# Kernel tuning notes

Measured on AMD Instinct MI355X. Metric: run time of the kernel, lower is better.

## Reference

```python
import jax, jax.numpy as jnp
import numpy as np

N_NODES = 100000
N_EDGES = 1000000
N_GRAPHS = 4096
F_IN = 9
H = 64


def setup_inputs() -> dict:
    key = jax.random.key(0)
    ks = jax.random.split(key, 12)
    x = jax.random.normal(ks[0], (N_NODES, F_IN), dtype=jnp.float32)
    edge_index = jax.random.randint(ks[1], (2, N_EDGES), 0, N_NODES, dtype=jnp.int64)
    batch = jnp.sort(jax.random.randint(ks[2], (N_NODES,), 0, N_GRAPHS, dtype=jnp.int64))
    def lin(k, fan_in, fan_out):
        s = 1.0 / np.sqrt(fan_in)
        return jax.random.uniform(k, (fan_in, fan_out), jnp.float32, -s, s)
    return {
        "x": x, "edge_index": edge_index, "batch": batch,
        "W1": lin(ks[3], F_IN, H), "b1": jnp.zeros((H,), jnp.float32),
        "W2": lin(ks[4], H, H),    "b2": jnp.zeros((H,), jnp.float32),
        "W3": lin(ks[5], H, H),    "b3": jnp.zeros((H,), jnp.float32),
        "W4": lin(ks[6], H, H),    "b4": jnp.zeros((H,), jnp.float32),
        "Wout": lin(ks[7], H, 1),  "bout": jnp.zeros((1,), jnp.float32),
    }


def reference(x, edge_index, batch, W1, b1, W2, b2, W3, b3, W4, b4, Wout, bout):
    N = x.shape[0]
    loops = jnp.arange(N, dtype=edge_index.dtype)
    src = jnp.concatenate([edge_index[0], loops])  # messages flow src -> dst (PyG source_to_target)
    dst = jnp.concatenate([edge_index[1], loops])
    # symmetric GCN normalization with self-loops: deg includes self-loop
    deg = jax.ops.segment_sum(jnp.ones_like(dst, dtype=x.dtype), dst, num_segments=N)
    dis = jax.lax.rsqrt(jnp.maximum(deg, 1.0))  # deg >= 1 thanks to self-loops
    norm = dis[src] * dis[dst]                  # [E+N]

    def gcn_conv(h, W, b):
        h = h @ W                                # transform first (PyG order)
        msgs = h[src] * norm[:, None]            # [E+N, H]
        return jax.ops.segment_sum(msgs, dst, num_segments=N) + b

    h = jax.nn.relu(gcn_conv(x, W1, b1))
    h = jax.nn.relu(gcn_conv(h, W2, b2))
    h = jax.nn.relu(gcn_conv(h, W3, b3))
    h = jax.nn.relu(gcn_conv(h, W4, b4))

    # global mean pool over graphs
    sums = jax.ops.segment_sum(h, batch, num_segments=N_GRAPHS)      # [G, H]
    counts = jax.ops.segment_sum(jnp.ones((N,), h.dtype), batch, num_segments=N_GRAPHS)
    pooled = sums / jnp.maximum(counts, 1.0)[:, None]
    return pooled @ Wout + bout                  # [G, 1]
```

## Files before the change

### kernel.cpp

```cpp
#include <hip/hip_runtime.h>
#include <hip/hip_fp16.h>


static inline size_t align256(size_t x){ return (x + 255) & ~size_t(255); }

#define CHUNK 2048
#define SCAP  3072

struct __align__(8)  h4v { __half2 a, b; };
struct __align__(16) h8v { __half2 a, b, c, d; };

typedef _Float16 f16x8 __attribute__((ext_vector_type(8)));
typedef float    f32x4 __attribute__((ext_vector_type(4)));

__global__ __launch_bounds__(256) void k_sortchunk(
    const int* __restrict__ src, const int* __restrict__ dst,
    int* __restrict__ binned, int* __restrict__ hoffC, int E){
  __shared__ int hcnt[1024];
  __shared__ int simg[CHUNK];
  int c = blockIdx.x, t = threadIdx.x;
  int e0 = c*CHUNK;
  int cnt = E - e0; if (cnt > CHUNK) cnt = CHUNK;

  for (int i = t; i < 1024; i += 256) hcnt[i] = 0;
  __syncthreads();

  int b_[8], r_[8], v_[8];
  #pragma unroll
  for (int j = 0; j < 8; j++){
    int i = t + j*256;
    if (i < cnt){
      int d = dst[e0+i];
      int s = src[e0+i];
      int b = d >> 7;
      b_[j] = b;
      r_[j] = atomicAdd(&hcnt[b], 1);
      v_[j] = (s << 7) | (d & 127);
    } else b_[j] = -1;
  }
  __syncthreads();

  int own[4];
  #pragma unroll
  for (int j = 0; j < 4; j++) own[j] = hcnt[t + j*256];
  for (int off = 1; off < 1024; off <<= 1){
    int nv[4];
    #pragma unroll
    for (int j = 0; j < 4; j++){
      int i = t + j*256;
      nv[j] = hcnt[i] + ((i >= off) ? hcnt[i-off] : 0);
    }
    __syncthreads();
    #pragma unroll
    for (int j = 0; j < 4; j++) hcnt[t + j*256] = nv[j];
    __syncthreads();
  }
  #pragma unroll
  for (int j = 0; j < 4; j++) hcnt[t + j*256] -= own[j];
  __syncthreads();

  for (int i = t; i < 783; i += 256) hoffC[c*783 + i] = hcnt[i];

  #pragma unroll
  for (int j = 0; j < 8; j++)
    if (b_[j] >= 0) simg[hcnt[b_[j]] + r_[j]] = v_[j];
  __syncthreads();

  for (int i = t; i < cnt; i += 256) binned[e0 + i] = simg[i];
}

__global__ __launch_bounds__(256) void k_bktsum(
    const int* __restrict__ hoffC, int* __restrict__ btot,
    float* __restrict__ gsum, int NC, int NBK, int G){
  __shared__ int s[256];
  int b = blockIdx.x, t = threadIdx.x;
  int gid = b*256 + t;
  if (gid < G) gsum[gid] = 0.f;
  int tot = 0;
  for (int c = t; c < NC; c += 256)
    tot += hoffC[c*783 + b + 1] - hoffC[c*783 + b];
  s[t] = tot; __syncthreads();
  for (int off = 128; off > 0; off >>= 1){
    if (t < off) s[t] += s[t+off];
    __syncthreads();
  }
  if (t == 0) btot[b] = s[0];
}

__global__ __launch_bounds__(1024) void k_bktscan(
    const int* __restrict__ btot, int* __restrict__ bbase,
    int* __restrict__ row_ptr, int NBK, int N, int E){
  __shared__ int s[1024];
  int t = threadIdx.x;
  int v = (t < NBK) ? btot[t] : 0;
  s[t] = v; __syncthreads();
  for (int off = 1; off < 1024; off <<= 1){
    int add = (t >= off) ? s[t-off] : 0; __syncthreads();
    s[t] += add; __syncthreads();
  }
  if (t < NBK) bbase[t] = s[t] - v;
  if (t == 0) row_ptr[N] = E;
}

__global__ __launch_bounds__(256) void k_gather2(
    const int* __restrict__ binned, const int* __restrict__ hoffC,
    const int* __restrict__ bbase, const float* __restrict__ x,
    int* __restrict__ row_ptr, float* __restrict__ dis,
    float* __restrict__ xs, int* __restrict__ csr, int N, int NC){
  __shared__ int lcur[128];
  __shared__ int lscan[128];
  __shared__ float ldis[128];
  __shared__ int stage[SCAP];
  __shared__ int scount;
  int b = blockIdx.x, t = threadIdx.x;
  int n0 = b << 7;
  int nn = N - n0; if (nn > 128) nn = 128;
  if (t < 128) lcur[t] = 0;
  if (t == 0) scount = 0;
  __syncthreads();
  for (int c = t; c < NC; c += 256){
    int o0 = hoffC[c*783 + b];
    int o1 = hoffC[c*783 + b + 1];
    int len = o1 - o0;
    if (len > 0){
      int base = atomicAdd(&scount, len);
      int sbase = c*CHUNK;
      for (int k = 0; k < len; k++){
        int v = binned[sbase + o0 + k];
        atomicAdd(&lcur[v & 127], 1);
        int pos = base + k;
        if (pos < SCAP) stage[pos] = v;
      }
    }
  }
  __syncthreads();
  int degv = (t < 128) ? lcur[t] : 0;
  if (t < 128) lscan[t] = degv;
  __syncthreads();
  for (int off = 1; off < 128; off <<= 1){
    int add = (t < 128 && t >= off) ? lscan[t-off] : 0;
    __syncthreads();
    if (t < 128) lscan[t] += add;
    __syncthreads();
  }
  int bb = bbase[b];
  if (t < nn){
    int row = bb + lscan[t] - degv;
    row_ptr[n0 + t] = row;
    float dv = rsqrtf((float)(degv + 1));
    dis[n0 + t] = dv;
    ldis[t] = dv;
    lcur[t] = row;
  }
  __syncthreads();
  for (int i = t; i < nn*9; i += 256)
    xs[(size_t)n0*9 + i] = x[(size_t)n0*9 + i] * ldis[i/9];
  int sc = scount;
  if (sc <= SCAP){
    for (int i = t; i < sc; i += 256){
      int v = stage[i];
      int pos = atomicAdd(&lcur[v & 127], 1);
      csr[pos] = v >> 7;
    }
  } else {
    for (int c = t; c < NC; c += 256){
      int o0 = hoffC[c*783 + b];
      int o1 = hoffC[c*783 + b + 1];
      int sbase = c*CHUNK;
      for (int k = o0; k < o1; k++){
        int v = binned[sbase + k];
        int pos = atomicAdd(&lcur[v & 127], 1);
        csr[pos] = v >> 7;
      }
    }
  }
}

__global__ void k_agg9(const float* __restrict__ xs, const float* __restrict__ dis,
                       const int* __restrict__ row_ptr, const int* __restrict__ csr,
                       float* __restrict__ xagg, int N){
  int tid = blockIdx.x*blockDim.x + threadIdx.x;
  if (tid >= N*9) return;
  int n = tid/9, f = tid - n*9;
  float dn = dis[n];
  int s0 = row_ptr[n], s1 = row_ptr[n+1];
  float a0 = xs[tid];
  float a1 = 0.f, a2 = 0.f, a3 = 0.f;
  int j = s0;
  for (; j + 3 < s1; j += 4){
    int e0 = csr[j], e1 = csr[j+1], e2 = csr[j+2], e3 = csr[j+3];
    a0 += xs[e0*9+f];
    a1 += xs[e1*9+f];
    a2 += xs[e2*9+f];
    a3 += xs[e3*9+f];
  }
  for (; j < s1; j++) a0 += xs[csr[j]*9+f];
  xagg[tid] = ((a0+a1)+(a2+a3))*dn;
}

__device__ __forceinline__ void mfma_epilogue(
    const _Float16* hlw, const f16x8 (&wf)[4][2],
    __half* __restrict__ mo, int wid, int nwaves, int N, int lane){
  int lm = lane & 15, lk = lane >> 4;
  f16x8 hb0 = *(const f16x8*)(hlw + lm*72 + lk*8);
  f16x8 hb1 = *(const f16x8*)(hlw + lm*72 + 32 + lk*8);
  int node = wid + lm*nwaves;
  bool ok = (node < N);
  __half* row = mo + (size_t)node*64;
  #pragma unroll
  for (int ft = 0; ft < 4; ft++){
    f32x4 acc = {0.f, 0.f, 0.f, 0.f};
    acc = __builtin_amdgcn_mfma_f32_16x16x32_f16(wf[ft][0], hb0, acc, 0, 0, 0);
    acc = __builtin_amdgcn_mfma_f32_16x16x32_f16(wf[ft][1], hb1, acc, 0, 0, 0);
    if (ok){
      h4v o;
      o.a = __floats2half2_rn(acc[0], acc[1]);
      o.b = __floats2half2_rn(acc[2], acc[3]);
      *(h4v*)(row + ft*16 + lk*4) = o;
    }
  }
}

#define LOAD_WFRAGS(Wn)                                                    \
  f16x8 wf[4][2];                                                          \
  { int lm_ = lane & 15, lk_ = lane >> 4;                                  \
    _Pragma("unroll") for (int ft = 0; ft < 4; ft++)                       \
    _Pragma("unroll") for (int kb = 0; kb < 2; kb++)                       \
    _Pragma("unroll") for (int j = 0; j < 8; j++)                          \
      wf[ft][kb][j] = (_Float16)Wn[(kb*32 + lk_*8 + j)*64 + ft*16 + lm_]; }

__global__ __launch_bounds__(256) void k_lin1_fused(
    const float* __restrict__ xagg, const float* __restrict__ W1,
    const float* __restrict__ b1, const float* __restrict__ dis,
    const float* __restrict__ W2, __half* __restrict__ mo, int N, int nwaves){
  __shared__ float W1l[576];
  __shared__ float b1l[64];
  __shared__ _Float16 hl[4][16*72];
  int t = threadIdx.x;
  for (int i = t; i < 576; i += 256) W1l[i] = W1[i];
  if (t < 64) b1l[t] = b1[t];
  __syncthreads();
  int lane = t & 63, w = t >> 6;
  int wid = (blockIdx.x*blockDim.x + t) >> 6;
  LOAD_WFRAGS(W2)
  _Float16* hlw = hl[w];
  for (int i = 0; i < 16; i++){
    int n = wid + i*nwaves;
    _Float16 hv = (_Float16)0.f;
    if (n < N){
      float acc = b1l[lane];
      #pragma unroll
      for (int k = 0; k < 9; k++) acc = fmaf(xagg[n*9+k], W1l[k*64+lane], acc);
      hv = (_Float16)(fmaxf(acc, 0.f) * dis[n]);
    }
    hlw[i*72 + lane] = hv;
  }
  mfma_epilogue(hlw, wf, mo, wid, nwaves, N, lane);
}

#define ACC8(g_)  do{ float2 t_;                                   \
  t_ = __half22float2((g_).a); acc0 += t_.x; acc1 += t_.y;         \
  t_ = __half22float2((g_).b); acc2 += t_.x; acc3 += t_.y;         \
  t_ = __half22float2((g_).c); acc4 += t_.x; acc5 += t_.y;         \
  t_ = __half22float2((g_).d); acc6 += t_.x; acc7 += t_.y; }while(0)

#define RED3(v)  do{ v += __shfl_xor(v, 8,64);                     \
                     v += __shfl_xor(v,16,64);                     \
                     v += __shfl_xor(v,32,64); }while(0)

#define AGG_ISSUE(n_, rp0_, rp1_, rn0_, rn1_, e0_, e1_, g0_, g1_, sf_, dn_) \
  do{                                                                      \
    int nn_ = (n_) + 2*nwaves;                                             \
    rn0_ = 0; rn1_ = 0;                                                    \
    if (nn_ < N){ rn0_ = row_ptr[nn_]; rn1_ = row_ptr[nn_+1]; }            \
    e0_ = -1; e1_ = -1;                                                    \
    if ((n_) < N){                                                         \
      sf_ = m[(size_t)(n_)*8 + q2];                                        \
      dn_ = dis[n_];                                                       \
      int j0_ = (rp0_) + sub, j1_ = (rp0_) + 8 + sub;                      \
      if (j0_ < (rp1_)) e0_ = csr[j0_];                                    \
      if (j1_ < (rp1_)) e1_ = csr[j1_];                                    \
      if (e0_ >= 0) g0_ = m[(size_t)e0_*8 + q2];                           \
      if (e1_ >= 0) g1_ = m[(size_t)e1_*8 + q2];                           \
    }                                                                      \
  }while(0)

#define AGG_ACCRED(n_, rp0_, rp1_, e0_, e1_, g0_, g1_, sf_, dn_)           \
      float acc0=0.f,acc1=0.f,acc2=0.f,acc3=0.f;                           \
      float acc4=0.f,acc5=0.f,acc6=0.f,acc7=0.f;                           \
      if (e0_ >= 0) ACC8(g0_);                                             \
      if (e1_ >= 0) ACC8(g1_);                                             \
      for (int j_ = (rp0_) + 16 + sub; j_ < (rp1_); j_ += 8){              \
        h8v gx_ = m[(size_t)csr[j_]*8 + q2]; ACC8(gx_);                    \
      }                                                                    \
      RED3(acc0); RED3(acc1); RED3(acc2); RED3(acc3);                      \
      RED3(acc4); RED3(acc5); RED3(acc6); RED3(acc7);                      \
      float2 s01=__half22float2((sf_).a), s23=__half22float2((sf_).b);     \
      float2 s45=__half22float2((sf_).c), s67=__half22float2((sf_).d);     \
      float r0 = fmaxf(fmaf(acc0 + s01.x, dn_, bb0.x), 0.f);               \
      float r1 = fmaxf(fmaf(acc1 + s01.y, dn_, bb0.y), 0.f);               \
      float r2 = fmaxf(fmaf(acc2 + s23.x, dn_, bb0.z), 0.f);               \
      float r3 = fmaxf(fmaf(acc3 + s23.y, dn_, bb0.w), 0.f);               \
      float r4 = fmaxf(fmaf(acc4 + s45.x, dn_, bb1.x), 0.f);               \
      float r5 = fmaxf(fmaf(acc5 + s45.y, dn_, bb1.y), 0.f);               \
      float r6 = fmaxf(fmaf(acc6 + s67.x, dn_, bb1.z), 0.f);               \
      float r7 = fmaxf(fmaf(acc7 + s67.y, dn_, bb1.w), 0.f);

#define AGG_REDUCE(n_, rp0_, rp1_, e0_, e1_, g0_, g1_, sf_, dn_, i_)       \
  do{                                                                      \
    if ((n_) < N){                                                         \
      AGG_ACCRED(n_, rp0_, rp1_, e0_, e1_, g0_, g1_, sf_, dn_)             \
      if (sub == 0){                                                       \
        h8v hv_;                                                           \
        hv_.a = __floats2half2_rn(r0*(dn_), r1*(dn_));                     \
        hv_.b = __floats2half2_rn(r2*(dn_), r3*(dn_));                     \
        hv_.c = __floats2half2_rn(r4*(dn_), r5*(dn_));                     \
        hv_.d = __floats2half2_rn(r6*(dn_), r7*(dn_));                     \
        *(h8v*)(hlw + (i_)*72 + q2*8) = hv_;                               \
      }                                                                    \
    } else if (sub == 0){                                                  \
      h8v z_; z_.a = __floats2half2_rn(0.f, 0.f);                          \
      z_.b = z_.a; z_.c = z_.a; z_.d = z_.a;                               \
      *(h8v*)(hlw + (i_)*72 + q2*8) = z_;                                  \
    }                                                                      \
  }while(0)

#define OUT_ISSUE(n_, rp0_, rp1_, rn0_, rn1_, e0_, e1_, g0_, g1_, sf_, dn_, bg_) \
  do{                                                                      \
    int pn_ = (n_) + nwaves;                                               \
    rn0_ = 0; rn1_ = 0;                                                    \
    if (pn_ < N){ rn0_ = row_ptr[pn_]; rn1_ = row_ptr[pn_+1]; }            \
    sf_ = m[(size_t)(n_)*8 + q2];                                          \
    dn_ = dis[n_];                                                         \
    bg_ = batch[n_];                                                       \
    e0_ = -1; e1_ = -1;                                                    \
    int j0_ = (rp0_) + sub, j1_ = (rp0_) + 8 + sub;                        \
    if (j0_ < (rp1_)) e0_ = csr[j0_];                                      \
    if (j1_ < (rp1_)) e1_ = csr[j1_];                                      \
    if (e0_ >= 0) g0_ = m[(size_t)e0_*8 + q2];                             \
    if (e1_ >= 0) g1_ = m[(size_t)e1_*8 + q2];                             \
  }while(0)

#define OUT_REDUCE(n_, rp0_, rp1_, e0_, e1_, g0_, g1_, sf_, dn_, bg_)      \
  do{                                                                      \
    float4 bb0 = b4[q2*2], bb1 = b4[q2*2+1];                               \
    float4 w0 = wo4[q2*2], w1 = wo4[q2*2+1];                               \
    AGG_ACCRED(n_, rp0_, rp1_, e0_, e1_, g0_, g1_, sf_, dn_)               \
    float p_ = r0*w0.x + r1*w0.y + r2*w0.z + r3*w0.w                       \
             + r4*w1.x + r5*w1.y + r6*w1.z + r7*w1.w;                      \
    p_ += __shfl_xor(p_,1,64); p_ += __shfl_xor(p_,2,64);                  \
    p_ += __shfl_xor(p_,4,64);                                             \
    if (lane == 0) atomicAdd(&gsum[bg_], p_);                              \
  }while(0)

__global__ __launch_bounds__(256) void k_agg_fused(
    const h8v* __restrict__ m, const float* __restrict__ dis,
    const float* __restrict__ b, const float* __restrict__ Wn,
    const int* __restrict__ row_ptr, const int* __restrict__ csr,
    __half* __restrict__ mo, int N, int nwaves){
  __shared__ _Float16 hl[4][16*72];
  int t = threadIdx.x;
  int lane = t & 63, w = t >> 6;
  int sub = lane >> 3, q2 = lane & 7;
  int wid = (blockIdx.x*blockDim.x + t) >> 6;
  _Float16* hlw = hl[w];
  const float4* b4 = (const float4*)b;
  float4 bb0 = b4[q2*2], bb1 = b4[q2*2+1];

  int nA = wid,          rA0 = 0, rA1 = 0;
  int nB = wid + nwaves, rB0 = 0, rB1 = 0;
  if (nA < N){ rA0 = row_ptr[nA]; rA1 = row_ptr[nA+1]; }
  if (nB < N){ rB0 = row_ptr[nB]; rB1 = row_ptr[nB+1]; }
  int eA0, eA1, eB0, eB1, rnA0, rnA1, rnB0, rnB1;
  h8v gA0, gA1, sfA, gB0, gB1, sfB;
  float dnA = 0.f, dnB = 0.f;
  AGG_ISSUE(nA, rA0, rA1, rnA0, rnA1, eA0, eA1, gA0, gA1, sfA, dnA);
  for (int p = 0; p < 8; p++){
    AGG_ISSUE(nB, rB0, rB1, rnB0, rnB1, eB0, eB1, gB0, gB1, sfB, dnB);
    AGG_REDUCE(nA, rA0, rA1, eA0, eA1, gA0, gA1, sfA, dnA, 2*p);
    nA += 2*nwaves; rA0 = rnA0; rA1 = rnA1;
    if (p < 7)
      AGG_ISSUE(nA, rA0, rA1, rnA0, rnA1, eA0, eA1, gA0, gA1, sfA, dnA);
    AGG_REDUCE(nB, rB0, rB1, eB0, eB1, gB0, gB1, sfB, dnB, 2*p+1);
    nB += 2*nwaves; rB0 = rnB0; rB1 = rnB1;
  }
  LOAD_WFRAGS(Wn)
  mfma_epilogue(hlw, wf, mo, wid, nwaves, N, lane);
}

__global__ __launch_bounds__(256) void k_agg64_out(
    const h8v* __restrict__ m, const float* __restrict__ dis,
    const float* __restrict__ b, const float* __restrict__ Wout,
    const int* __restrict__ batch,
    const int* __restrict__ row_ptr, const int* __restrict__ csr,
    float* gsum, int N, int nwaves){
  int lane = threadIdx.x & 63;
  int sub = lane >> 3, q2 = lane & 7;
  int wid = (blockIdx.x*blockDim.x + threadIdx.x) >> 6;
  if (wid >= N) return;
  const float4* b4 = (const float4*)b;
  const float4* wo4 = (const float4*)Wout;

  int nA = wid;
  int rA0 = row_ptr[nA], rA1 = row_ptr[nA+1];
  int rnA0, rnA1, rnB0, rnB1;
  int eA0, eA1, eB0, eB1, bgA, bgB;
  h8v gA0, gA1, sfA, gB0, gB1, sfB;
  float dnA, dnB;
  int rB0, rB1;
  OUT_ISSUE(nA, rA0, rA1, rnA0, rnA1, eA0, eA1, gA0, gA1, sfA, dnA, bgA);
  for(;;){
    int nB = nA + nwaves;
    if (nB < N){
      rB0 = rnA0; rB1 = rnA1;
      OUT_ISSUE(nB, rB0, rB1, rnB0, rnB1, eB0, eB1, gB0, gB1, sfB, dnB, bgB);
    }
    OUT_REDUCE(nA, rA0, rA1, eA0, eA1, gA0, gA1, sfA, dnA, bgA);
    if (nB >= N) return;
    int nA2 = nB + nwaves;
    if (nA2 < N){
      nA = nA2;
      rA0 = rnB0; rA1 = rnB1;
      OUT_ISSUE(nA, rA0, rA1, rnA0, rnA1, eA0, eA1, gA0, gA1, sfA, dnA, bgA);
    }
    OUT_REDUCE(nB, rB0, rB1, eB0, eB1, gB0, gB1, sfB, dnB, bgB);
    if (nA2 >= N) return;
  }
}

__global__ void k_final(const float* __restrict__ gsum, const int* __restrict__ batch,
                        const float* __restrict__ bout, float* __restrict__ out,
                        int G, int N){
  int g = blockIdx.x*blockDim.x + threadIdx.x;
  if (g >= G) return;
  int lo = 0, hi = N;
  while (lo < hi){ int mid = (lo+hi)>>1; if (batch[mid] <  g) lo = mid+1; else hi = mid; }
  int lb = lo;
  lo = 0; hi = N;
  while (lo < hi){ int mid = (lo+hi)>>1; if (batch[mid] <= g) lo = mid+1; else hi = mid; }
  int c = lo - lb;
  out[g] = gsum[g]/(float)(c > 0 ? c : 1) + bout[0];
}

extern "C" void kernel_launch(void* const* d_in, const int* in_sizes, int n_in,
                              void* d_out, int out_size, void* d_ws, size_t ws_size,
                              hipStream_t stream){
  const float* x    = (const float*)d_in[0];
  const int*   ei   = (const int*)d_in[1];
  const int*   batch= (const int*)d_in[2];
  const float* W1 = (const float*)d_in[3];  const float* b1 = (const float*)d_in[4];
  const float* W2 = (const float*)d_in[5];  const float* b2 = (const float*)d_in[6];
  const float* W3 = (const float*)d_in[7];  const float* b3 = (const float*)d_in[8];
  const float* W4 = (const float*)d_in[9];  const float* b4 = (const float*)d_in[10];
  const float* Wout = (const float*)d_in[11]; const float* bout = (const float*)d_in[12];
  float* out = (float*)d_out;

  const int N = in_sizes[0]/9;
  const int E = in_sizes[1]/2;
  const int G = out_size;
  const int* src = ei;
  const int* dst = ei + E;

  char* ws = (char*)d_ws;
  size_t off = 0;
  auto alloc = [&](size_t bytes){ void* p = ws + off; off = align256(off + bytes); return p; };
  int*   row_ptr  = (int*)  alloc((size_t)(N+1)*4);
  int*   csr      = (int*)  alloc((size_t)E*4);
  float* dis      = (float*)alloc((size_t)N*4);
  const int NBK = (N + 127)/128;
  const int NC  = (E + CHUNK-1)/CHUNK;
  int*   hoffC    = (int*)  alloc((size_t)NC*783*4);
  int*   btot     = (int*)  alloc((size_t)NBK*4);
  int*   bbase    = (int*)  alloc((size_t)NBK*4);
  float* gsum     = (float*)alloc((size_t)G*4);
  __half* mA      = (__half*)alloc((size_t)N*64*2);
  __half* mB      = (__half*)alloc((size_t)N*64*2);
  int*   binned   = (int*)mA;
  float* xs       = (float*)mB;
  float* xagg     = xs + (size_t)N*9;

  const int AGG_BLOCKS = 2048;
  const int AGG_WAVES  = AGG_BLOCKS*4;

  k_sortchunk<<<NC, 256, 0, stream>>>(src, dst, binned, hoffC, E);
  k_bktsum   <<<NBK, 256, 0, stream>>>(hoffC, btot, gsum, NC, NBK, G);
  k_bktscan  <<<1, 1024, 0, stream>>>(btot, bbase, row_ptr, NBK, N, E);
  k_gather2  <<<NBK, 256, 0, stream>>>(binned, hoffC, bbase, x,
                                       row_ptr, dis, xs, csr, N, NC);

  k_agg9  <<<(N*9+255)/256, 256, 0, stream>>>(xs, dis, row_ptr, csr, xagg, N);
  k_lin1_fused<<<AGG_BLOCKS, 256, 0, stream>>>(xagg, W1, b1, dis, W2, mA, N, AGG_WAVES);

  k_agg_fused<<<AGG_BLOCKS, 256, 0, stream>>>((const h8v*)mA, dis, b2, W3,
                                              row_ptr, csr, mB, N, AGG_WAVES);
  k_agg_fused<<<AGG_BLOCKS, 256, 0, stream>>>((const h8v*)mB, dis, b3, W4,
                                              row_ptr, csr, mA, N, AGG_WAVES);
  k_agg64_out<<<AGG_BLOCKS, 256, 0, stream>>>((const h8v*)mA, dis, b4, Wout, batch,
                                              row_ptr, csr, gsum, N, AGG_WAVES);

  k_final<<<(G+255)/256, 256, 0, stream>>>(gsum, batch, bout, out, G, N);
}
```

Measured before the change: 301.9 us.

## Fold bucket scan into gather, double sort chunk, restructure output-layer pipelining

Doubles the edge-sort chunk size so each sort block bins two 2048-edge halves. This halves the number of chunks the bucket-sum and gather kernels must walk per bucket. Removes the single-block bucket-scan kernel: each gather block now computes its own base offset by reducing the btot prefix itself, saving a launch at the cost of redundant prefix reads. The final aggregation/readout kernel swaps its two-node unrolled prefetch for a simpler loop that prefetches CSR indices one node ahead and row pointers two ahead. Neighbour feature gathers are now issued in the same iteration, which may expose more gather latency.

```diff
diff --git a/kernel.cpp b/kernel.cpp
--- a/kernel.cpp
+++ b/kernel.cpp
@@ -4,7 +4,7 @@
 
 static inline size_t align256(size_t x){ return (x + 255) & ~size_t(255); }
 
-#define CHUNK 2048
+#define CHUNK 4096
 #define SCAP  3072
 
 struct __align__(8)  h4v { __half2 a, b; };
@@ -25,7 +25,7 @@
   for (int i = t; i < 1024; i += 256) hcnt[i] = 0;
   __syncthreads();
 
-  int b_[8], r_[8], v_[8];
+  int bA[8], rA[8], vA[8], bB[8], rB[8], vB[8];
   #pragma unroll
   for (int j = 0; j < 8; j++){
     int i = t + j*256;
@@ -33,10 +33,22 @@
       int d = dst[e0+i];
       int s = src[e0+i];
       int b = d >> 7;
-      b_[j] = b;
-      r_[j] = atomicAdd(&hcnt[b], 1);
-      v_[j] = (s << 7) | (d & 127);
-    } else b_[j] = -1;
+      bA[j] = b;
+      rA[j] = atomicAdd(&hcnt[b], 1);
+      vA[j] = (s << 7) | (d & 127);
+    } else bA[j] = -1;
+  }
+  #pragma unroll
+  for (int j = 0; j < 8; j++){
+    int i = t + 2048 + j*256;
+    if (i < cnt){
+      int d = dst[e0+i];
+      int s = src[e0+i];
+      int b = d >> 7;
+      bB[j] = b;
+      rB[j] = atomicAdd(&hcnt[b], 1);
+      vB[j] = (s << 7) | (d & 127);
+    } else bB[j] = -1;
   }
   __syncthreads();
 
@@ -63,7 +75,10 @@
 
   #pragma unroll
   for (int j = 0; j < 8; j++)
-    if (b_[j] >= 0) simg[hcnt[b_[j]] + r_[j]] = v_[j];
+    if (bA[j] >= 0) simg[hcnt[bA[j]] + rA[j]] = vA[j];
+  #pragma unroll
+  for (int j = 0; j < 8; j++)
+    if (bB[j] >= 0) simg[hcnt[bB[j]] + rB[j]] = vB[j];
   __syncthreads();
 
   for (int i = t; i < cnt; i += 256) binned[e0 + i] = simg[i];
@@ -87,37 +102,34 @@
   if (t == 0) btot[b] = s[0];
 }
 
-__global__ __launch_bounds__(1024) void k_bktscan(
-    const int* __restrict__ btot, int* __restrict__ bbase,
-    int* __restrict__ row_ptr, int NBK, int N, int E){
-  __shared__ int s[1024];
-  int t = threadIdx.x;
-  int v = (t < NBK) ? btot[t] : 0;
-  s[t] = v; __syncthreads();
-  for (int off = 1; off < 1024; off <<= 1){
-    int add = (t >= off) ? s[t-off] : 0; __syncthreads();
-    s[t] += add; __syncthreads();
-  }
-  if (t < NBK) bbase[t] = s[t] - v;
-  if (t == 0) row_ptr[N] = E;
-}
-
 __global__ __launch_bounds__(256) void k_gather2(
     const int* __restrict__ binned, const int* __restrict__ hoffC,
-    const int* __restrict__ bbase, const float* __restrict__ x,
+    const int* __restrict__ btot, const float* __restrict__ x,
     int* __restrict__ row_ptr, float* __restrict__ dis,
-    float* __restrict__ xs, int* __restrict__ csr, int N, int NC){
+    float* __restrict__ xs, int* __restrict__ csr, int N, int NC, int E){
   __shared__ int lcur[128];
   __shared__ int lscan[128];
   __shared__ float ldis[128];
   __shared__ int stage[SCAP];
   __shared__ int scount;
+  __shared__ int sbb;
   int b = blockIdx.x, t = threadIdx.x;
   int n0 = b << 7;
   int nn = N - n0; if (nn > 128) nn = 128;
+
+  int psum = 0;
+  for (int i = t; i < b; i += 256) psum += btot[i];
+  stage[t] = psum; __syncthreads();
+  for (int off = 128; off > 0; off >>= 1){
+    if (t < off) stage[t] += stage[t+off];
+    __syncthreads();
+  }
+  if (t == 0) sbb = stage[0];
+  if (t == 0 && b == 0) row_ptr[N] = E;
   if (t < 128) lcur[t] = 0;
   if (t == 0) scount = 0;
   __syncthreads();
+
   for (int c = t; c < NC; c += 256){
     int o0 = hoffC[c*783 + b];
     int o1 = hoffC[c*783 + b + 1];
@@ -143,7 +155,7 @@
     if (t < 128) lscan[t] += add;
     __syncthreads();
   }
-  int bb = bbase[b];
+  int bb = sbb;
   if (t < nn){
     int row = bb + lscan[t] - degv;
     row_ptr[n0 + t] = row;
@@ -325,34 +337,6 @@
     }                                                                      \
   }while(0)
 
-#define OUT_ISSUE(n_, rp0_, rp1_, rn0_, rn1_, e0_, e1_, g0_, g1_, sf_, dn_, bg_) \
-  do{                                                                      \
-    int pn_ = (n_) + nwaves;                                               \
-    rn0_ = 0; rn1_ = 0;                                                    \
-    if (pn_ < N){ rn0_ = row_ptr[pn_]; rn1_ = row_ptr[pn_+1]; }            \
-    sf_ = m[(size_t)(n_)*8 + q2];                                          \
-    dn_ = dis[n_];                                                         \
-    bg_ = batch[n_];                                                       \
-    e0_ = -1; e1_ = -1;                                                    \
-    int j0_ = (rp0_) + sub, j1_ = (rp0_) + 8 + sub;                        \
-    if (j0_ < (rp1_)) e0_ = csr[j0_];                                      \
-    if (j1_ < (rp1_)) e1_ = csr[j1_];                                      \
-    if (e0_ >= 0) g0_ = m[(size_t)e0_*8 + q2];                             \
-    if (e1_ >= 0) g1_ = m[(size_t)e1_*8 + q2];                             \
-  }while(0)
-
-#define OUT_REDUCE(n_, rp0_, rp1_, e0_, e1_, g0_, g1_, sf_, dn_, bg_)      \
-  do{                                                                      \
-    float4 bb0 = b4[q2*2], bb1 = b4[q2*2+1];                               \
-    float4 w0 = wo4[q2*2], w1 = wo4[q2*2+1];                               \
-    AGG_ACCRED(n_, rp0_, rp1_, e0_, e1_, g0_, g1_, sf_, dn_)               \
-    float p_ = r0*w0.x + r1*w0.y + r2*w0.z + r3*w0.w                       \
-             + r4*w1.x + r5*w1.y + r6*w1.z + r7*w1.w;                      \
-    p_ += __shfl_xor(p_,1,64); p_ += __shfl_xor(p_,2,64);                  \
-    p_ += __shfl_xor(p_,4,64);                                             \
-    if (lane == 0) atomicAdd(&gsum[bg_], p_);                              \
-  }while(0)
-
 __global__ __launch_bounds__(256) void k_agg_fused(
     const h8v* __restrict__ m, const float* __restrict__ dis,
     const float* __restrict__ b, const float* __restrict__ Wn,
@@ -396,35 +380,46 @@
     float* gsum, int N, int nwaves){
   int lane = threadIdx.x & 63;
   int sub = lane >> 3, q2 = lane & 7;
-  int wid = (blockIdx.x*blockDim.x + threadIdx.x) >> 6;
-  if (wid >= N) return;
+  int n = (blockIdx.x*blockDim.x + threadIdx.x) >> 6;
+  if (n >= N) return;
   const float4* b4 = (const float4*)b;
   const float4* wo4 = (const float4*)Wout;
-
-  int nA = wid;
-  int rA0 = row_ptr[nA], rA1 = row_ptr[nA+1];
-  int rnA0, rnA1, rnB0, rnB1;
-  int eA0, eA1, eB0, eB1, bgA, bgB;
-  h8v gA0, gA1, sfA, gB0, gB1, sfB;
-  float dnA, dnB;
-  int rB0, rB1;
-  OUT_ISSUE(nA, rA0, rA1, rnA0, rnA1, eA0, eA1, gA0, gA1, sfA, dnA, bgA);
-  for(;;){
-    int nB = nA + nwaves;
-    if (nB < N){
-      rB0 = rnA0; rB1 = rnA1;
-      OUT_ISSUE(nB, rB0, rB1, rnB0, rnB1, eB0, eB1, gB0, gB1, sfB, dnB, bgB);
-    }
-    OUT_REDUCE(nA, rA0, rA1, eA0, eA1, gA0, gA1, sfA, dnA, bgA);
-    if (nB >= N) return;
-    int nA2 = nB + nwaves;
-    if (nA2 < N){
-      nA = nA2;
-      rA0 = rnB0; rA1 = rnB1;
-      OUT_ISSUE(nA, rA0, rA1, rnA0, rnA1, eA0, eA1, gA0, gA1, sfA, dnA, bgA);
-    }
-    OUT_REDUCE(nB, rB0, rB1, eB0, eB1, gB0, gB1, sfB, dnB, bgB);
-    if (nA2 >= N) return;
+  float4 bb0 = b4[q2*2], bb1 = b4[q2*2+1];
+  float4 w0 = wo4[q2*2], w1 = wo4[q2*2+1];
+
+  int rp0 = row_ptr[n], rp1 = row_ptr[n+1];
+  int n1 = n + nwaves;
+  int rq0 = 0, rq1 = 0;
+  if (n1 < N){ rq0 = row_ptr[n1]; rq1 = row_ptr[n1+1]; }
+  int e0 = -1, e1 = -1;
+  { int j0 = rp0 + sub, j1 = rp0 + 8 + sub;
+    if (j0 < rp1) e0 = csr[j0];
+    if (j1 < rp1) e1 = csr[j1]; }
+  while (true){
+    h8v g0, g1, sf;
+    if (e0 >= 0) g0 = m[(size_t)e0*8 + q2];
+    if (e1 >= 0) g1 = m[(size_t)e1*8 + q2];
+    sf = m[(size_t)n*8 + q2];
+    float dn = dis[n];
+    int bg = batch[n];
+    int n2 = n1 + nwaves;
+    int rr0 = 0, rr1 = 0;
+    if (n2 < N){ rr0 = row_ptr[n2]; rr1 = row_ptr[n2+1]; }
+    int f0 = -1, f1 = -1;
+    if (n1 < N){
+      int j0 = rq0 + sub, j1 = rq0 + 8 + sub;
+      if (j0 < rq1) f0 = csr[j0];
+      if (j1 < rq1) f1 = csr[j1];
+    }
+    AGG_ACCRED(n, rp0, rp1, e0, e1, g0, g1, sf, dn)
+    float p = r0*w0.x + r1*w0.y + r2*w0.z + r3*w0.w
+            + r4*w1.x + r5*w1.y + r6*w1.z + r7*w1.w;
+    p += __shfl_xor(p,1,64); p += __shfl_xor(p,2,64); p += __shfl_xor(p,4,64);
+    if (lane == 0) atomicAdd(&gsum[bg], p);
+    if (n1 >= N) break;
+    n = n1; rp0 = rq0; rp1 = rq1;
+    n1 = n2; rq0 = rr0; rq1 = rr1;
+    e0 = f0; e1 = f1;
   }
 }
 
@@ -471,7 +466,6 @@
   const int NC  = (E + CHUNK-1)/CHUNK;
   int*   hoffC    = (int*)  alloc((size_t)NC*783*4);
   int*   btot     = (int*)  alloc((size_t)NBK*4);
-  int*   bbase    = (int*)  alloc((size_t)NBK*4);
   float* gsum     = (float*)alloc((size_t)G*4);
   __half* mA      = (__half*)alloc((size_t)N*64*2);
   __half* mB      = (__half*)alloc((size_t)N*64*2);
@@ -484,9 +478,8 @@
 
   k_sortchunk<<<NC, 256, 0, stream>>>(src, dst, binned, hoffC, E);
   k_bktsum   <<<NBK, 256, 0, stream>>>(hoffC, btot, gsum, NC, NBK, G);
-  k_bktscan  <<<1, 1024, 0, stream>>>(btot, bbase, row_ptr, NBK, N, E);
-  k_gather2  <<<NBK, 256, 0, stream>>>(binned, hoffC, bbase, x,
-                                       row_ptr, dis, xs, csr, N, NC);
+  k_gather2  <<<NBK, 256, 0, stream>>>(binned, hoffC, btot, x,
+                                       row_ptr, dis, xs, csr, N, NC, E);
 
   k_agg9  <<<(N*9+255)/256, 256, 0, stream>>>(xs, dis, row_ptr, csr, xagg, N);
   k_lin1_fused<<<AGG_BLOCKS, 256, 0, stream>>>(xagg, W1, b1, dis, W2, mA, N, AGG_WAVES);
```

Result: no change. 299.7 us (-0.7%).
